# Performance work log

Hardware: AMD Instinct MI355X
Metric: run time of the kernel (lower is better)

The kernel has to match this reference:

```python
import jax, jax.numpy as jnp
import numpy as np

MAX_DISTANCE = 9          # search radius (pixels, at half resolution)
PAD_VAL = 1e10            # padding value; sigmoid saturates to 1 exactly as with 1e20,
                          # but avoids inf in fp32 squared sums (same output, safe grads)


def _offsets(m):
    k = 2 * m + 1
    offs = np.stack(np.meshgrid(np.arange(k), np.arange(k), indexing='ij'), -1)
    return jnp.asarray(offs.reshape(-1, 2))  # [K,2], row-major (dy, dx) like torch unfold


def _interp_matrix(out_size, in_size):
    # 1-D bilinear interpolation matrix, align_corners=True (matches F.interpolate)
    scale = (in_size - 1) / (out_size - 1)
    pos = jnp.arange(out_size, dtype=jnp.float32) * scale
    lo = jnp.clip(jnp.floor(pos).astype(jnp.int32), 0, in_size - 2)
    frac = pos - lo.astype(jnp.float32)
    rows = jnp.arange(out_size)
    M = jnp.zeros((out_size, in_size), jnp.float32)
    return M.at[rows, lo].add(1.0 - frac).at[rows, lo + 1].add(frac)


def _local_distances(query, prev, m):
    # local_pairwise_distances2 with MODEL_LOCAL_DOWNSAMPLE=True
    H, W, C = query.shape
    x = query.reshape(H // 2, 2, W // 2, 2, C).mean(axis=(1, 3))  # avg_pool2d 2x2
    y = prev.reshape(H // 2, 2, W // 2, 2, C).mean(axis=(1, 3))
    h, w = H // 2, W // 2
    ypad = jnp.pad(y, ((m, m), (m, m), (0, 0)), constant_values=PAD_VAL)
    offs = _offsets(m)

    def one(off):
        sl = jax.lax.dynamic_slice(ypad, (off[0], off[1], 0), (h, w, C))
        return jnp.sum((x - sl) ** 2, axis=-1)  # [h,w]

    d = jax.vmap(one)(offs)                      # [K,h,w]
    d = (jax.nn.sigmoid(d) - 0.5) * 2.0
    d = jnp.transpose(d, (1, 2, 0))              # [h,w,K]
    Mh = _interp_matrix(H, h)
    Mw = _interp_matrix(W, w)
    return jnp.einsum('Hh,Ww,hwk->HWk', Mh, Mw, d)  # bilinear upsample


def setup_inputs() -> dict:
    key = jax.random.key(0)
    k1, k2, k3 = jax.random.split(key, 3)
    H, W, C, n_objs = 96, 160, 100, 3
    return {
        'prev_frame_embedding': jax.random.normal(k1, (H, W, C), jnp.float32),
        'query_embedding': jax.random.normal(k2, (H, W, C), jnp.float32),
        'prev_frame_labels': jax.random.randint(k3, (H, W, 1), 0, n_objs).astype(jnp.int32),
        'gt_ids': jnp.arange(n_objs, dtype=jnp.int32),
    }


def reference(prev_frame_embedding, query_embedding, prev_frame_labels, gt_ids):
    m = MAX_DISTANCE
    H, W, _ = prev_frame_embedding.shape
    n = gt_ids.shape[0]
    d = _local_distances(query_embedding, prev_frame_embedding, m)  # [H,W,K]

    masks = prev_frame_labels == gt_ids[None, None, :]  # [H,W,n] bool
    mpad = jnp.pad(masks, ((m, m), (m, m), (0, 0)))      # pad False
    offs = _offsets(m)

    def one(off):
        return jax.lax.dynamic_slice(mpad, (off[0], off[1], 0), (H, W, n))

    om = jnp.transpose(jax.vmap(one)(offs), (1, 2, 0, 3))  # [H,W,K,n]
    d_masked = jnp.where(om, d[..., None], 1.0)
    dists = jnp.min(d_masked, axis=2)                      # [H,W,n]
    return dists.reshape(1, H, W, n, 1)
```

## Files before the change

kernel.cpp:

```cpp
#include <hip/hip_runtime.h>
#include <hip/hip_bf16.h>
#include <math.h>

#define HF 96
#define WF 160
#define CH 100
#define HH 48
#define HW 80
#define NPIX 3840
#define MD 9
#define KD 19
#define K2 361
#define NMAX 8

#define OFF_XT 0
#define OFF_YT (CH*NPIX)
#define OFF_XS (2*CH*NPIX)
#define OFF_YS (2*CH*NPIX + NPIX)
#define OFF_DH (2*CH*NPIX + 2*NPIX)

__global__ __launch_bounds__(256) void pool_kernel(
    const float* __restrict__ q, const float* __restrict__ p,
    float* __restrict__ Xt, float* __restrict__ Yt,
    float* __restrict__ xs, float* __restrict__ ys) {
  int w = threadIdx.x >> 6, L = threadIdx.x & 63;
  int pix = blockIdx.x * 4 + w;
  int i = pix / HW, j = pix - i * HW;
  int base = (2 * i) * WF * CH + (2 * j) * CH;
  float nx = 0.f, ny = 0.f;
  for (int c = L; c < CH; c += 64) {
    int b = base + c;
    float xv = 0.25f * (q[b] + q[b + CH] + q[b + WF * CH] + q[b + WF * CH + CH]);
    float yv = 0.25f * (p[b] + p[b + CH] + p[b + WF * CH] + p[b + WF * CH + CH]);
    Xt[c * NPIX + pix] = xv;
    Yt[c * NPIX + pix] = yv;
    nx = fmaf(xv, xv, nx);
    ny = fmaf(yv, yv, ny);
  }
  for (int s = 32; s > 0; s >>= 1) {
    nx += __shfl_down(nx, s);
    ny += __shfl_down(ny, s);
  }
  if (L == 0) { xs[pix] = nx; ys[pix] = ny; }
}

__global__ __launch_bounds__(128) void dist_kernel(
    const float* __restrict__ Xt, const float* __restrict__ Yt,
    const float* __restrict__ xs, const float* __restrict__ ys,
    __hip_bfloat16* __restrict__ dh2) {
  int t = blockIdx.x * 128 + threadIdx.x;
  int u = blockIdx.y;
  int dp = u >> 1, h = u & 1;
  int ip = t / HW, j = t - ip * HW;
  int iA = 2 * ip;
  int pixA = iA * HW + j, pixB = pixA + HW;

  bool doA = (dp < KD);
  bool doB = (dp >= 1);
  int r = iA + dp - MD;
  bool rowOK = (r >= 0 && r < HH);
  int cbase = j - MD + 10 * h;
  int nd = h ? 9 : 10;
  int kbA = dp * KD + 10 * h;
  int kbB = (dp - 1) * KD + 10 * h;

  if (!rowOK) {
    __hip_bfloat16 one = __float2bfloat16(1.0f);
#pragma unroll
    for (int d = 0; d < 10; ++d) {
      if (d >= nd) break;
      if (doA) dh2[(kbA + d) * NPIX + pixA] = one;
      if (doB) dh2[(kbB + d) * NPIX + pixB] = one;
    }
    return;
  }

  float accA[10], accB[10];
#pragma unroll
  for (int d = 0; d < 10; ++d) { accA[d] = 0.f; accB[d] = 0.f; }

  const float* xpA = Xt + pixA;
  const float* xpB = Xt + pixB;
  const float* yp  = Yt + r * HW + cbase;
#pragma unroll 2
  for (int c = 0; c < CH; ++c) {
    float xa = *xpA, xb = *xpB;
#pragma unroll
    for (int d = 0; d < 10; ++d) {
      float yv = yp[d];
      accA[d] = fmaf(xa, yv, accA[d]);
      accB[d] = fmaf(xb, yv, accB[d]);
    }
    xpA += NPIX; xpB += NPIX; yp += NPIX;
  }

  float xssA = xs[pixA];
  float xssB = xs[pixB];
  const float* ysr = ys + r * HW;
#pragma unroll
  for (int d = 0; d < 10; ++d) {
    if (d >= nd) break;
    int jj = cbase + d;
    bool okc = (jj >= 0) && (jj < HW);
    int jcl = jj < 0 ? 0 : (jj > HW - 1 ? HW - 1 : jj);
    float yss = ysr[jcl];
    if (doA) {
      float s = xssA + yss - 2.f * accA[d];
      float e = __expf(-s);
      float rv = okc ? (1.f - e) / (1.f + e) : 1.0f;
      dh2[(kbA + d) * NPIX + pixA] = __float2bfloat16(rv);
    }
    if (doB) {
      float s = xssB + yss - 2.f * accB[d];
      float e = __expf(-s);
      float rv = okc ? (1.f - e) / (1.f + e) : 1.0f;
      dh2[(kbB + d) * NPIX + pixB] = __float2bfloat16(rv);
    }
  }
}

template <int N>
__global__ __launch_bounds__(1024) void upmin_kernel(
    const __hip_bfloat16* __restrict__ dh2, const int* __restrict__ labels,
    const int* __restrict__ gt, float* __restrict__ out) {
  int w = threadIdx.x >> 6;
  int lane = threadIdx.x & 63;
  int pixel = blockIdx.x * 64 + lane;
  int I = pixel / WF, J = pixel - I * WF;

  const float sy = (float)((HH - 1.0) / (HF - 1.0));
  const float sx = (float)((HW - 1.0) / (WF - 1.0));
  float py = (float)I * sy;
  int y0 = (int)floorf(py); if (y0 > HH - 2) y0 = HH - 2; if (y0 < 0) y0 = 0;
  float fy = py - (float)y0;
  float px = (float)J * sx;
  int x0 = (int)floorf(px); if (x0 > HW - 2) x0 = HW - 2; if (x0 < 0) x0 = 0;
  float fx = px - (float)x0;
  float w00 = (1.f - fy) * (1.f - fx), w01 = (1.f - fy) * fx;
  float w10 = fy * (1.f - fx),         w11 = fy * fx;
  int np00 = y0 * HW + x0;

  int gtl[N];
  float mins[N];
#pragma unroll
  for (int o = 0; o < N; ++o) { gtl[o] = gt[o]; mins[o] = 1.0f; }

  for (int k = w; k < K2; k += 16) {
    int dy = k / KD, dx = k - dy * KD;
    int P = I + dy - MD, Q = J + dx - MD;
    const __hip_bfloat16* dk = dh2 + k * NPIX + np00;
    float v = w00 * __bfloat162float(dk[0]) + w01 * __bfloat162float(dk[1]) +
              w10 * __bfloat162float(dk[HW]) + w11 * __bfloat162float(dk[HW + 1]);
    if (P >= 0 && P < HF && Q >= 0 && Q < WF) {
      int lab = labels[P * WF + Q];
#pragma unroll
      for (int o = 0; o < N; ++o)
        if (lab == gtl[o]) mins[o] = fminf(mins[o], v);
    }
  }

  __shared__ float mm[16][64][N];
#pragma unroll
  for (int o = 0; o < N; ++o) mm[w][lane][o] = mins[o];
  __syncthreads();
  if (w < 8) {
#pragma unroll
    for (int o = 0; o < N; ++o)
      mm[w][lane][o] = fminf(mm[w][lane][o], mm[w + 8][lane][o]);
  }
  __syncthreads();
  if (w < 4) {
#pragma unroll
    for (int o = 0; o < N; ++o)
      mm[w][lane][o] = fminf(mm[w][lane][o], mm[w + 4][lane][o]);
  }
  __syncthreads();
  if (w == 0) {
#pragma unroll
    for (int o = 0; o < N; ++o) {
      float m = fminf(fminf(mm[0][lane][o], mm[1][lane][o]),
                      fminf(mm[2][lane][o], mm[3][lane][o]));
      out[pixel * N + o] = m;
    }
  }
}

extern "C" void kernel_launch(void* const* d_in, const int* in_sizes, int n_in,
                              void* d_out, int out_size, void* d_ws, size_t ws_size,
                              hipStream_t stream) {
  const float* prev  = (const float*)d_in[0];
  const float* query = (const float*)d_in[1];
  const int* labels  = (const int*)d_in[2];
  const int* gt      = (const int*)d_in[3];
  int n = in_sizes[3];
  if (n > NMAX) n = NMAX;
  float* ws = (float*)d_ws;
  float* Xt = ws + OFF_XT;
  float* Yt = ws + OFF_YT;
  float* xs = ws + OFF_XS;
  float* ys = ws + OFF_YS;
  __hip_bfloat16* dh2 = (__hip_bfloat16*)(ws + OFF_DH);
  float* out = (float*)d_out;

  hipLaunchKernelGGL(pool_kernel, dim3(NPIX / 4), dim3(256), 0, stream,
                     query, prev, Xt, Yt, xs, ys);
  hipLaunchKernelGGL(dist_kernel, dim3(1920 / 128, 40), dim3(128), 0, stream,
                     Xt, Yt, xs, ys, dh2);
  dim3 ug(HF * WF / 64), ub(1024);
  switch (n) {
    case 1: hipLaunchKernelGGL(upmin_kernel<1>, ug, ub, 0, stream, dh2, labels, gt, out); break;
    case 2: hipLaunchKernelGGL(upmin_kernel<2>, ug, ub, 0, stream, dh2, labels, gt, out); break;
    case 3: hipLaunchKernelGGL(upmin_kernel<3>, ug, ub, 0, stream, dh2, labels, gt, out); break;
    case 4: hipLaunchKernelGGL(upmin_kernel<4>, ug, ub, 0, stream, dh2, labels, gt, out); break;
    case 5: hipLaunchKernelGGL(upmin_kernel<5>, ug, ub, 0, stream, dh2, labels, gt, out); break;
    case 6: hipLaunchKernelGGL(upmin_kernel<6>, ug, ub, 0, stream, dh2, labels, gt, out); break;
    case 7: hipLaunchKernelGGL(upmin_kernel<7>, ug, ub, 0, stream, dh2, labels, gt, out); break;
    default: hipLaunchKernelGGL(upmin_kernel<8>, ug, ub, 0, stream, dh2, labels, gt, out); break;
  }
}
```

Before: 115.2 us.

## Fuse pool, distance and upsample-min into one cooperative persistent kernel

```diff
diff --git a/kernel.cpp b/kernel.cpp
--- a/kernel.cpp
+++ b/kernel.cpp
@@ -1,6 +1,9 @@
 #include <hip/hip_runtime.h>
 #include <hip/hip_bf16.h>
+#include <hip/hip_cooperative_groups.h>
 #include <math.h>
+
+namespace cg = cooperative_groups;
 
 #define HF 96
 #define WF 160
@@ -19,168 +22,178 @@
 #define OFF_YS (2*CH*NPIX + NPIX)
 #define OFF_DH (2*CH*NPIX + 2*NPIX)
 
-__global__ __launch_bounds__(256) void pool_kernel(
+#define NBLK 600
+#define NTHR 256
+#define NWAVE (NBLK * 4)
+
+template <int N>
+__global__ __launch_bounds__(256, 3) void fused_kernel(
     const float* __restrict__ q, const float* __restrict__ p,
     float* __restrict__ Xt, float* __restrict__ Yt,
-    float* __restrict__ xs, float* __restrict__ ys) {
-  int w = threadIdx.x >> 6, L = threadIdx.x & 63;
-  int pix = blockIdx.x * 4 + w;
-  int i = pix / HW, j = pix - i * HW;
-  int base = (2 * i) * WF * CH + (2 * j) * CH;
-  float nx = 0.f, ny = 0.f;
-  for (int c = L; c < CH; c += 64) {
-    int b = base + c;
-    float xv = 0.25f * (q[b] + q[b + CH] + q[b + WF * CH] + q[b + WF * CH + CH]);
-    float yv = 0.25f * (p[b] + p[b + CH] + p[b + WF * CH] + p[b + WF * CH + CH]);
-    Xt[c * NPIX + pix] = xv;
-    Yt[c * NPIX + pix] = yv;
-    nx = fmaf(xv, xv, nx);
-    ny = fmaf(yv, yv, ny);
-  }
-  for (int s = 32; s > 0; s >>= 1) {
-    nx += __shfl_down(nx, s);
-    ny += __shfl_down(ny, s);
-  }
-  if (L == 0) { xs[pix] = nx; ys[pix] = ny; }
-}
-
-__global__ __launch_bounds__(128) void dist_kernel(
-    const float* __restrict__ Xt, const float* __restrict__ Yt,
-    const float* __restrict__ xs, const float* __restrict__ ys,
-    __hip_bfloat16* __restrict__ dh2) {
-  int t = blockIdx.x * 128 + threadIdx.x;
-  int u = blockIdx.y;
-  int dp = u >> 1, h = u & 1;
-  int ip = t / HW, j = t - ip * HW;
-  int iA = 2 * ip;
-  int pixA = iA * HW + j, pixB = pixA + HW;
-
-  bool doA = (dp < KD);
-  bool doB = (dp >= 1);
-  int r = iA + dp - MD;
-  bool rowOK = (r >= 0 && r < HH);
-  int cbase = j - MD + 10 * h;
-  int nd = h ? 9 : 10;
-  int kbA = dp * KD + 10 * h;
-  int kbB = (dp - 1) * KD + 10 * h;
-
-  if (!rowOK) {
-    __hip_bfloat16 one = __float2bfloat16(1.0f);
-#pragma unroll
-    for (int d = 0; d < 10; ++d) {
-      if (d >= nd) break;
-      if (doA) dh2[(kbA + d) * NPIX + pixA] = one;
-      if (doB) dh2[(kbB + d) * NPIX + pixB] = one;
-    }
-    return;
-  }
-
-  float accA[10], accB[10];
-#pragma unroll
-  for (int d = 0; d < 10; ++d) { accA[d] = 0.f; accB[d] = 0.f; }
-
-  const float* xpA = Xt + pixA;
-  const float* xpB = Xt + pixB;
-  const float* yp  = Yt + r * HW + cbase;
+    float* __restrict__ xs, float* __restrict__ ys,
+    __hip_bfloat16* __restrict__ dh2,
+    const int* __restrict__ labels, const int* __restrict__ gt,
+    float* __restrict__ out) {
+  cg::grid_group grid = cg::this_grid();
+  __shared__ float ex[128][21];
+  __shared__ float mm[4][64][N];
+
+  {
+    int w = threadIdx.x >> 6, L = threadIdx.x & 63;
+    int wg = blockIdx.x * 4 + w;
+    for (int pix = wg; pix < NPIX; pix += NWAVE) {
+      int i = pix / HW, j = pix - i * HW;
+      int base = (2 * i) * WF * CH + (2 * j) * CH;
+      float nx = 0.f, ny = 0.f;
+      for (int c = L; c < CH; c += 64) {
+        int b = base + c;
+        float xv = 0.25f * (q[b] + q[b + CH] + q[b + WF * CH] + q[b + WF * CH + CH]);
+        float yv = 0.25f * (p[b] + p[b + CH] + p[b + WF * CH] + p[b + WF * CH + CH]);
+        Xt[c * NPIX + pix] = xv;
+        Yt[c * NPIX + pix] = yv;
+        nx = fmaf(xv, xv, nx);
+        ny = fmaf(yv, yv, ny);
+      }
+      for (int s = 32; s > 0; s >>= 1) {
+        nx += __shfl_down(nx, s);
+        ny += __shfl_down(ny, s);
+      }
+      if (L == 0) { xs[pix] = nx; ys[pix] = ny; }
+    }
+  }
+  grid.sync();
+
+  {
+    int half = threadIdx.x >> 7;
+    int il = threadIdx.x & 127;
+    int item = blockIdx.x * 128 + il;
+    int t = item % 1920, u = item / 1920;
+    int dp = u >> 1, h = u & 1;
+    int ip = t / HW, j = t - ip * HW;
+    int iA = 2 * ip;
+    int pixA = iA * HW + j, pixB = pixA + HW;
+
+    bool doA = (dp < KD);
+    bool doB = (dp >= 1);
+    int r = iA + dp - MD;
+    bool rowOK = (r >= 0 && r < HH);
+    int cbase = j - MD + 10 * h;
+    int nd = h ? 9 : 10;
+    int kbA = dp * KD + 10 * h;
+    int kbB = (dp - 1) * KD + 10 * h;
+
+    float accA[10], accB[10];
+#pragma unroll
+    for (int d = 0; d < 10; ++d) { accA[d] = 0.f; accB[d] = 0.f; }
+
+    if (rowOK) {
+      int c0 = half * 50;
+      const float* xpA = Xt + c0 * NPIX + pixA;
+      const float* xpB = Xt + c0 * NPIX + pixB;
+      const float* yp  = Yt + c0 * NPIX + r * HW + cbase;
 #pragma unroll 2
-  for (int c = 0; c < CH; ++c) {
-    float xa = *xpA, xb = *xpB;
-#pragma unroll
-    for (int d = 0; d < 10; ++d) {
-      float yv = yp[d];
-      accA[d] = fmaf(xa, yv, accA[d]);
-      accB[d] = fmaf(xb, yv, accB[d]);
-    }
-    xpA += NPIX; xpB += NPIX; yp += NPIX;
-  }
-
-  float xssA = xs[pixA];
-  float xssB = xs[pixB];
-  const float* ysr = ys + r * HW;
-#pragma unroll
-  for (int d = 0; d < 10; ++d) {
-    if (d >= nd) break;
-    int jj = cbase + d;
-    bool okc = (jj >= 0) && (jj < HW);
-    int jcl = jj < 0 ? 0 : (jj > HW - 1 ? HW - 1 : jj);
-    float yss = ysr[jcl];
-    if (doA) {
-      float s = xssA + yss - 2.f * accA[d];
-      float e = __expf(-s);
-      float rv = okc ? (1.f - e) / (1.f + e) : 1.0f;
-      dh2[(kbA + d) * NPIX + pixA] = __float2bfloat16(rv);
-    }
-    if (doB) {
-      float s = xssB + yss - 2.f * accB[d];
-      float e = __expf(-s);
-      float rv = okc ? (1.f - e) / (1.f + e) : 1.0f;
-      dh2[(kbB + d) * NPIX + pixB] = __float2bfloat16(rv);
-    }
-  }
-}
-
-template <int N>
-__global__ __launch_bounds__(1024) void upmin_kernel(
-    const __hip_bfloat16* __restrict__ dh2, const int* __restrict__ labels,
-    const int* __restrict__ gt, float* __restrict__ out) {
-  int w = threadIdx.x >> 6;
-  int lane = threadIdx.x & 63;
-  int pixel = blockIdx.x * 64 + lane;
-  int I = pixel / WF, J = pixel - I * WF;
-
-  const float sy = (float)((HH - 1.0) / (HF - 1.0));
-  const float sx = (float)((HW - 1.0) / (WF - 1.0));
-  float py = (float)I * sy;
-  int y0 = (int)floorf(py); if (y0 > HH - 2) y0 = HH - 2; if (y0 < 0) y0 = 0;
-  float fy = py - (float)y0;
-  float px = (float)J * sx;
-  int x0 = (int)floorf(px); if (x0 > HW - 2) x0 = HW - 2; if (x0 < 0) x0 = 0;
-  float fx = px - (float)x0;
-  float w00 = (1.f - fy) * (1.f - fx), w01 = (1.f - fy) * fx;
-  float w10 = fy * (1.f - fx),         w11 = fy * fx;
-  int np00 = y0 * HW + x0;
-
-  int gtl[N];
-  float mins[N];
-#pragma unroll
-  for (int o = 0; o < N; ++o) { gtl[o] = gt[o]; mins[o] = 1.0f; }
-
-  for (int k = w; k < K2; k += 16) {
-    int dy = k / KD, dx = k - dy * KD;
-    int P = I + dy - MD, Q = J + dx - MD;
-    const __hip_bfloat16* dk = dh2 + k * NPIX + np00;
-    float v = w00 * __bfloat162float(dk[0]) + w01 * __bfloat162float(dk[1]) +
-              w10 * __bfloat162float(dk[HW]) + w11 * __bfloat162float(dk[HW + 1]);
-    if (P >= 0 && P < HF && Q >= 0 && Q < WF) {
-      int lab = labels[P * WF + Q];
-#pragma unroll
-      for (int o = 0; o < N; ++o)
-        if (lab == gtl[o]) mins[o] = fminf(mins[o], v);
-    }
-  }
-
-  __shared__ float mm[16][64][N];
-#pragma unroll
-  for (int o = 0; o < N; ++o) mm[w][lane][o] = mins[o];
-  __syncthreads();
-  if (w < 8) {
-#pragma unroll
-    for (int o = 0; o < N; ++o)
-      mm[w][lane][o] = fminf(mm[w][lane][o], mm[w + 8][lane][o]);
-  }
-  __syncthreads();
-  if (w < 4) {
-#pragma unroll
-    for (int o = 0; o < N; ++o)
-      mm[w][lane][o] = fminf(mm[w][lane][o], mm[w + 4][lane][o]);
-  }
-  __syncthreads();
-  if (w == 0) {
-#pragma unroll
-    for (int o = 0; o < N; ++o) {
-      float m = fminf(fminf(mm[0][lane][o], mm[1][lane][o]),
-                      fminf(mm[2][lane][o], mm[3][lane][o]));
-      out[pixel * N + o] = m;
+      for (int c = 0; c < 50; ++c) {
+        float xa = *xpA, xb = *xpB;
+#pragma unroll
+        for (int d = 0; d < 10; ++d) {
+          float yv = yp[d];
+          accA[d] = fmaf(xa, yv, accA[d]);
+          accB[d] = fmaf(xb, yv, accB[d]);
+        }
+        xpA += NPIX; xpB += NPIX; yp += NPIX;
+      }
+    }
+    if (half == 1) {
+#pragma unroll
+      for (int d = 0; d < 10; ++d) { ex[il][d] = accA[d]; ex[il][10 + d] = accB[d]; }
+    }
+    __syncthreads();
+    if (half == 0) {
+#pragma unroll
+      for (int d = 0; d < 10; ++d) { accA[d] += ex[il][d]; accB[d] += ex[il][10 + d]; }
+      if (!rowOK) {
+        __hip_bfloat16 one = __float2bfloat16(1.0f);
+#pragma unroll
+        for (int d = 0; d < 10; ++d) {
+          if (d >= nd) break;
+          if (doA) dh2[(kbA + d) * NPIX + pixA] = one;
+          if (doB) dh2[(kbB + d) * NPIX + pixB] = one;
+        }
+      } else {
+        float xssA = xs[pixA];
+        float xssB = xs[pixB];
+        const float* ysr = ys + r * HW;
+#pragma unroll
+        for (int d = 0; d < 10; ++d) {
+          if (d >= nd) break;
+          int jj = cbase + d;
+          bool okc = (jj >= 0) && (jj < HW);
+          int jcl = jj < 0 ? 0 : (jj > HW - 1 ? HW - 1 : jj);
+          float yss = ysr[jcl];
+          if (doA) {
+            float s = xssA + yss - 2.f * accA[d];
+            float e = __expf(-s);
+            float rv = okc ? (1.f - e) / (1.f + e) : 1.0f;
+            dh2[(kbA + d) * NPIX + pixA] = __float2bfloat16(rv);
+          }
+          if (doB) {
+            float s = xssB + yss - 2.f * accB[d];
+            float e = __expf(-s);
+            float rv = okc ? (1.f - e) / (1.f + e) : 1.0f;
+            dh2[(kbB + d) * NPIX + pixB] = __float2bfloat16(rv);
+          }
+        }
+      }
+    }
+  }
+  grid.sync();
+
+  if (blockIdx.x < (HF * WF / 64)) {
+    int w = threadIdx.x >> 6, lane = threadIdx.x & 63;
+    int pixel = blockIdx.x * 64 + lane;
+    int I = pixel / WF, J = pixel - I * WF;
+
+    const float sy = (float)((HH - 1.0) / (HF - 1.0));
+    const float sx = (float)((HW - 1.0) / (WF - 1.0));
+    float py = (float)I * sy;
+    int y0 = (int)floorf(py); if (y0 > HH - 2) y0 = HH - 2; if (y0 < 0) y0 = 0;
+    float fy = py - (float)y0;
+    float px = (float)J * sx;
+    int x0 = (int)floorf(px); if (x0 > HW - 2) x0 = HW - 2; if (x0 < 0) x0 = 0;
+    float fx = px - (float)x0;
+    float w00 = (1.f - fy) * (1.f - fx), w01 = (1.f - fy) * fx;
+    float w10 = fy * (1.f - fx),         w11 = fy * fx;
+    int np00 = y0 * HW + x0;
+
+    int gtl[N];
+    float mins[N];
+#pragma unroll
+    for (int o = 0; o < N; ++o) { gtl[o] = gt[o]; mins[o] = 1.0f; }
+
+    for (int k = w; k < K2; k += 4) {
+      int dy = k / KD, dx = k - dy * KD;
+      int P = I + dy - MD, Q = J + dx - MD;
+      const __hip_bfloat16* dk = dh2 + k * NPIX + np00;
+      float v = w00 * __bfloat162float(dk[0]) + w01 * __bfloat162float(dk[1]) +
+                w10 * __bfloat162float(dk[HW]) + w11 * __bfloat162float(dk[HW + 1]);
+      if (P >= 0 && P < HF && Q >= 0 && Q < WF) {
+        int lab = labels[P * WF + Q];
+#pragma unroll
+        for (int o = 0; o < N; ++o)
+          if (lab == gtl[o]) mins[o] = fminf(mins[o], v);
+      }
+    }
+
+#pragma unroll
+    for (int o = 0; o < N; ++o) mm[w][lane][o] = mins[o];
+    __syncthreads();
+    if (w == 0) {
+#pragma unroll
+      for (int o = 0; o < N; ++o) {
+        float m = fminf(fminf(mm[0][lane][o], mm[1][lane][o]),
+                        fminf(mm[2][lane][o], mm[3][lane][o]));
+        out[pixel * N + o] = m;
+      }
     }
   }
 }
@@ -202,19 +215,22 @@
   __hip_bfloat16* dh2 = (__hip_bfloat16*)(ws + OFF_DH);
   float* out = (float*)d_out;
 
-  hipLaunchKernelGGL(pool_kernel, dim3(NPIX / 4), dim3(256), 0, stream,
-                     query, prev, Xt, Yt, xs, ys);
-  hipLaunchKernelGGL(dist_kernel, dim3(1920 / 128, 40), dim3(128), 0, stream,
-                     Xt, Yt, xs, ys, dh2);
-  dim3 ug(HF * WF / 64), ub(1024);
+  void* args[10] = {
+    (void*)&query, (void*)&prev, (void*)&Xt, (void*)&Yt, (void*)&xs, (void*)&ys,
+    (void*)&dh2, (void*)&labels, (void*)&gt, (void*)&out };
+
+#define LAUNCH(NN) hipLaunchCooperativeKernel( \
+      reinterpret_cast<void*>(&fused_kernel<NN>), dim3(NBLK), dim3(NTHR), \
+      args, 0, stream)
   switch (n) {
-    case 1: hipLaunchKernelGGL(upmin_kernel<1>, ug, ub, 0, stream, dh2, labels, gt, out); break;
-    case 2: hipLaunchKernelGGL(upmin_kernel<2>, ug, ub, 0, stream, dh2, labels, gt, out); break;
-    case 3: hipLaunchKernelGGL(upmin_kernel<3>, ug, ub, 0, stream, dh2, labels, gt, out); break;
-    case 4: hipLaunchKernelGGL(upmin_kernel<4>, ug, ub, 0, stream, dh2, labels, gt, out); break;
-    case 5: hipLaunchKernelGGL(upmin_kernel<5>, ug, ub, 0, stream, dh2, labels, gt, out); break;
-    case 6: hipLaunchKernelGGL(upmin_kernel<6>, ug, ub, 0, stream, dh2, labels, gt, out); break;
-    case 7: hipLaunchKernelGGL(upmin_kernel<7>, ug, ub, 0, stream, dh2, labels, gt, out); break;
-    default: hipLaunchKernelGGL(upmin_kernel<8>, ug, ub, 0, stream, dh2, labels, gt, out); break;
-  }
+    case 1: LAUNCH(1); break;
+    case 2: LAUNCH(2); break;
+    case 3: LAUNCH(3); break;
+    case 4: LAUNCH(4); break;
+    case 5: LAUNCH(5); break;
+    case 6: LAUNCH(6); break;
+    case 7: LAUNCH(7); break;
+    default: LAUNCH(8); break;
+  }
+#undef LAUNCH
 }
```

Result: slower. 294.9 us (+155.9%).
